# Performance work log

Measured on AMD Instinct MI355X. Metric: run time of the kernel, lower is better.

Reference implementation:

```python
import jax, jax.numpy as jnp
import numpy as np

HIDDEN = 1024
NUM_HEADS = 16
HEAD_DIM = HIDDEN // NUM_HEADS


def setup_inputs() -> dict:
    key = jax.random.key(0)
    ks = jax.random.split(key, 11)
    s = 1.0 / np.sqrt(HIDDEN)
    x = jax.random.normal(ks[0], (4, 2048, HIDDEN), dtype=jnp.float32)
    Wq = jax.random.uniform(ks[1], (HIDDEN, HIDDEN), jnp.float32, -s, s)
    bq = jax.random.uniform(ks[2], (HIDDEN,), jnp.float32, -s, s)
    Wk = jax.random.uniform(ks[3], (HIDDEN, HIDDEN), jnp.float32, -s, s)
    bk = jax.random.uniform(ks[4], (HIDDEN,), jnp.float32, -s, s)
    Wv = jax.random.uniform(ks[5], (HIDDEN, HIDDEN), jnp.float32, -s, s)
    bv = jax.random.uniform(ks[6], (HIDDEN,), jnp.float32, -s, s)
    Wo = jax.random.uniform(ks[7], (HIDDEN, HIDDEN), jnp.float32, -s, s)
    bo = jax.random.uniform(ks[8], (HIDDEN,), jnp.float32, -s, s)
    ln_g = jnp.ones((HIDDEN,), jnp.float32)
    ln_b = jnp.zeros((HIDDEN,), jnp.float32)
    return {"x": x, "Wq": Wq, "bq": bq, "Wk": Wk, "bk": bk,
            "Wv": Wv, "bv": bv, "Wo": Wo, "bo": bo,
            "ln_g": ln_g, "ln_b": ln_b}


def _layer_norm(x, g, b, eps=1e-5):
    mu = jnp.mean(x, axis=-1, keepdims=True)
    var = jnp.var(x, axis=-1, keepdims=True)
    return (x - mu) * jax.lax.rsqrt(var + eps) * g + b


def reference(x, Wq, bq, Wk, bk, Wv, bv, Wo, bo, ln_g, ln_b):
    B, S, _ = x.shape
    residual = x
    h = _layer_norm(x, ln_g, ln_b)
    # projections (torch Linear: y = h @ W.T + b)
    q = (h @ Wq.T + bq).reshape(B, S, NUM_HEADS, HEAD_DIM).transpose(0, 2, 1, 3)
    k = (h @ Wk.T + bk).reshape(B, S, NUM_HEADS, HEAD_DIM).transpose(0, 2, 1, 3)
    v = (h @ Wv.T + bv).reshape(B, S, NUM_HEADS, HEAD_DIM).transpose(0, 2, 1, 3)
    scores = jnp.einsum('bhqd,bhkd->bhqk', q, k) / np.sqrt(HEAD_DIM).astype(np.float32)
    weights = jax.nn.softmax(scores, axis=-1)  # dropout = identity (eval mode)
    context = jnp.einsum('bhqk,bhkd->bhqd', weights, v)
    context = context.transpose(0, 2, 1, 3).reshape(B, S, HIDDEN)
    out = context @ Wo.T + bo
    return out + residual
```

## Files before the change

kernel.cpp:

```cpp
#include <hip/hip_runtime.h>

typedef unsigned short u16;
typedef unsigned int   u32;
using bf16x8 = __attribute__((ext_vector_type(8))) __bf16;
using f32x4  = __attribute__((ext_vector_type(4))) float;
using u32x2  = __attribute__((ext_vector_type(2))) unsigned int;

__device__ __forceinline__ u16 f2b(float f){
  union { float f; u32 i; } v; v.f = f;
  u32 r = v.i + 0x7FFFu + ((v.i >> 16) & 1u);
  return (u16)(r >> 16);
}
__device__ __forceinline__ u32 pk_bf16_trunc(float a, float b){
  return __builtin_amdgcn_perm(__float_as_uint(b), __float_as_uint(a), 0x07060302u);
}

__global__ __launch_bounds__(256) void pre_kernel(const float* __restrict__ x, const float* __restrict__ g,
                                                  const float* __restrict__ be, u16* __restrict__ h,
                                                  const float* __restrict__ s0, const float* __restrict__ s1,
                                                  const float* __restrict__ s2, const float* __restrict__ s3,
                                                  u16* __restrict__ wd){
  const int tid = threadIdx.x;
  if (blockIdx.x >= 8192){
    const int b2 = blockIdx.x - 8192;
    const float* srcs[4] = {s0, s1, s2, s3};
    const float* s = srcs[b2 >> 10];
    u16* dd = wd + (size_t)(b2 >> 10) * (1024u * 1024u);
    const int i = ((b2 & 1023) * 256 + tid) * 4;
    float4 v = *(const float4*)(s + i);
    uint2 o;
    o.x = (u32)f2b(v.x) | ((u32)f2b(v.y) << 16);
    o.y = (u32)f2b(v.z) | ((u32)f2b(v.w) << 16);
    *(uint2*)(dd + i) = o;
    return;
  }
  const int row = blockIdx.x;
  const float* xr = x + (size_t)row * 1024u;
  float4 raw = *(const float4*)(xr + tid * 4);
  float s  = raw.x + raw.y + raw.z + raw.w;
  float sq = raw.x*raw.x + raw.y*raw.y + raw.z*raw.z + raw.w*raw.w;
  #pragma unroll
  for (int m = 1; m < 64; m <<= 1){ s += __shfl_xor(s, m); sq += __shfl_xor(sq, m); }
  __shared__ float ws[4], wq[4];
  if ((tid & 63) == 0){ ws[tid >> 6] = s; wq[tid >> 6] = sq; }
  __syncthreads();
  s  = ws[0] + ws[1] + ws[2] + ws[3];
  sq = wq[0] + wq[1] + wq[2] + wq[3];
  const float mu = s * (1.0f / 1024.0f);
  const float rstd = rsqrtf(sq * (1.0f / 1024.0f) - mu * mu + 1e-5f);
  float4 gg = *(const float4*)(g + tid * 4);
  float4 bb = *(const float4*)(be + tid * 4);
  float y0 = (raw.x - mu) * rstd * gg.x + bb.x;
  float y1 = (raw.y - mu) * rstd * gg.y + bb.y;
  float y2 = (raw.z - mu) * rstd * gg.z + bb.z;
  float y3 = (raw.w - mu) * rstd * gg.w + bb.w;
  uint2 outv;
  outv.x = (u32)f2b(y0) | ((u32)f2b(y1) << 16);
  outv.y = (u32)f2b(y2) | ((u32)f2b(y3) << 16);
  *(uint2*)(h + (size_t)row * 1024u + tid * 4) = outv;
}

__global__ __launch_bounds__(256) void gemm_qkv(const u16* __restrict__ A, const u16* __restrict__ Wcat,
                                                const float* __restrict__ bq, const float* __restrict__ bk,
                                                const float* __restrict__ bv,
                                                u16* __restrict__ qo, u16* __restrict__ ko, u16* __restrict__ vt){
  __shared__ u16 lA[2][4096];
  __shared__ u16 lB[2][4096];
  const int tid = threadIdx.x;
  const int lane = tid & 63, wv = tid >> 6, l15 = lane & 15, quad = lane >> 4;
  const int wr = wv >> 1, wc = wv & 1;
  const int row0 = blockIdx.x * 128, col0 = blockIdx.y * 128;
  const int K = 1024;

  const int r0_ = tid >> 2,         c0_ = tid & 3;
  const int r1_ = (256 + tid) >> 2, c1_ = (256 + tid) & 3;
  const u16* Asrc0 = A    + (size_t)(row0 + r0_) * K + (c0_ ^ ((r0_ >> 1) & 3)) * 8;
  const u16* Asrc1 = A    + (size_t)(row0 + r1_) * K + (c1_ ^ ((r1_ >> 1) & 3)) * 8;
  const u16* Bsrc0 = Wcat + (size_t)(col0 + r0_) * K + (c0_ ^ ((r0_ >> 1) & 3)) * 8;
  const u16* Bsrc1 = Wcat + (size_t)(col0 + r1_) * K + (c1_ ^ ((r1_ >> 1) & 3)) * 8;
  const int cr = (quad ^ ((l15 >> 1) & 3)) * 8;

  f32x4 acc[4][4] = {};
  uint4 ar0, ar1, br0, br1;
  ar0 = *(const uint4*)(Asrc0);
  ar1 = *(const uint4*)(Asrc1);
  br0 = *(const uint4*)(Bsrc0);
  br1 = *(const uint4*)(Bsrc1);
  *(uint4*)&lA[0][tid * 8] = ar0;
  *(uint4*)&lA[0][(256 + tid) * 8] = ar1;
  *(uint4*)&lB[0][tid * 8] = br0;
  *(uint4*)&lB[0][(256 + tid) * 8] = br1;
  ar0 = *(const uint4*)(Asrc0 + 32);
  ar1 = *(const uint4*)(Asrc1 + 32);
  br0 = *(const uint4*)(Bsrc0 + 32);
  br1 = *(const uint4*)(Bsrc1 + 32);
  __syncthreads();

  for (int kt = 0; kt < 32; ++kt){
    const int cur = kt & 1;
    if (kt < 31){
      *(uint4*)&lA[cur ^ 1][tid * 8] = ar0;
      *(uint4*)&lA[cur ^ 1][(256 + tid) * 8] = ar1;
      *(uint4*)&lB[cur ^ 1][tid * 8] = br0;
      *(uint4*)&lB[cur ^ 1][(256 + tid) * 8] = br1;
    }
    if (kt < 30){
      const int o = (kt + 2) * 32;
      ar0 = *(const uint4*)(Asrc0 + o);
      ar1 = *(const uint4*)(Asrc1 + o);
      br0 = *(const uint4*)(Bsrc0 + o);
      br1 = *(const uint4*)(Bsrc1 + o);
    }
    bf16x8 af[4], bf[4];
    #pragma unroll
    for (int i = 0; i < 4; ++i) af[i] = *(const bf16x8*)&lA[cur][(wr * 64 + i * 16 + l15) * 32 + cr];
    #pragma unroll
    for (int j = 0; j < 4; ++j) bf[j] = *(const bf16x8*)&lB[cur][(wc * 64 + j * 16 + l15) * 32 + cr];
    #pragma unroll
    for (int i = 0; i < 4; ++i)
      #pragma unroll
      for (int j = 0; j < 4; ++j)
        acc[i][j] = __builtin_amdgcn_mfma_f32_16x16x32_bf16(af[i], bf[j], acc[i][j], 0, 0, 0);
    __syncthreads();
  }
  const int sel = col0 >> 10;
  if (sel < 2){
    const float* bias = (sel == 0) ? bq : bk;
    u16* dst = (sel == 0) ? qo : ko;
    #pragma unroll
    for (int i = 0; i < 4; ++i){
      const int grow = row0 + wr * 64 + i * 16 + quad * 4;
      #pragma unroll
      for (int j = 0; j < 4; ++j){
        const int gcol = (col0 & 1023) + wc * 64 + j * 16 + l15;
        const float bb = bias[gcol];
        #pragma unroll
        for (int r = 0; r < 4; ++r){
          size_t off = (size_t)(grow + r) * 1024u + gcol;
          dst[off] = f2b(acc[i][j][r] + bb);
        }
      }
    }
  } else {
    u16* pw = &lA[0][0] + wv * 2048;
    const int bglob = row0 >> 11;
    const int head  = ((col0 & 1023) >> 6) + wc;
    const int srem0 = (row0 & 2047) + wr * 64;
    const size_t vbase = (size_t)((bglob * 16 + head) * 64) * 2048u;
    #pragma unroll
    for (int p = 0; p < 2; ++p){
      #pragma unroll
      for (int i2 = 0; i2 < 2; ++i2){
        const int i = p * 2 + i2;
        #pragma unroll
        for (int j = 0; j < 4; ++j){
          const int d = j * 16 + l15;
          const float bv_ = bv[(col0 & 1023) + wc * 64 + d];
          const int u = (i2 * 4 + quad) ^ (d & 7);
          uint2 pk;
          pk.x = (u32)f2b(acc[i][j][0] + bv_) | ((u32)f2b(acc[i][j][1] + bv_) << 16);
          pk.y = (u32)f2b(acc[i][j][2] + bv_) | ((u32)f2b(acc[i][j][3] + bv_) << 16);
          *(uint2*)&pw[d * 32 + u * 4] = pk;
        }
      }
      const int dl = lane;
      #pragma unroll
      for (int c = 0; c < 4; ++c){
        const int u0 = (2 * c) ^ (dl & 7), u1 = (2 * c + 1) ^ (dl & 7);
        uint2 lo = *(const uint2*)&pw[dl * 32 + u0 * 4];
        uint2 hi = *(const uint2*)&pw[dl * 32 + u1 * 4];
        uint4 o4; o4.x = lo.x; o4.y = lo.y; o4.z = hi.x; o4.w = hi.y;
        *(uint4*)(vt + vbase + (size_t)dl * 2048u + srem0 + p * 32 + c * 8) = o4;
      }
    }
  }
}

__global__ __launch_bounds__(256) void gemm_out(const u16* __restrict__ A, const u16* __restrict__ W,
                                                const float* __restrict__ bias, const float* __restrict__ res,
                                                float* __restrict__ C, int M, int N, int K){
  __shared__ u16 lA[2][4096];
  __shared__ u16 lB[2][4096];
  const int tid = threadIdx.x;
  const int lane = tid & 63, wv = tid >> 6, l15 = lane & 15, quad = lane >> 4;
  const int wr = wv >> 1, wc = wv & 1;
  const int row0 = blockIdx.x * 128, col0 = blockIdx.y * 128;

  const int r0_ = tid >> 2,         c0_ = tid & 3;
  const int r1_ = (256 + tid) >> 2, c1_ = (256 + tid) & 3;
  const u16* Asrc0 = A + (size_t)(row0 + r0_) * K + (c0_ ^ ((r0_ >> 1) & 3)) * 8;
  const u16* Asrc1 = A + (size_t)(row0 + r1_) * K + (c1_ ^ ((r1_ >> 1) & 3)) * 8;
  const u16* Bsrc0 = W + (size_t)(col0 + r0_) * K + (c0_ ^ ((r0_ >> 1) & 3)) * 8;
  const u16* Bsrc1 = W + (size_t)(col0 + r1_) * K + (c1_ ^ ((r1_ >> 1) & 3)) * 8;
  const int cr = (quad ^ ((l15 >> 1) & 3)) * 8;

  f32x4 acc[4][4] = {};
  const int nkt = K >> 5;
  uint4 ar0, ar1, br0, br1;
  ar0 = *(const uint4*)(Asrc0);
  ar1 = *(const uint4*)(Asrc1);
  br0 = *(const uint4*)(Bsrc0);
  br1 = *(const uint4*)(Bsrc1);
  *(uint4*)&lA[0][tid * 8] = ar0;
  *(uint4*)&lA[0][(256 + tid) * 8] = ar1;
  *(uint4*)&lB[0][tid * 8] = br0;
  *(uint4*)&lB[0][(256 + tid) * 8] = br1;
  ar0 = *(const uint4*)(Asrc0 + 32);
  ar1 = *(const uint4*)(Asrc1 + 32);
  br0 = *(const uint4*)(Bsrc0 + 32);
  br1 = *(const uint4*)(Bsrc1 + 32);
  __syncthreads();

  for (int kt = 0; kt < nkt; ++kt){
    const int cur = kt & 1;
    if (kt < nkt - 1){
      *(uint4*)&lA[cur ^ 1][tid * 8] = ar0;
      *(uint4*)&lA[cur ^ 1][(256 + tid) * 8] = ar1;
      *(uint4*)&lB[cur ^ 1][tid * 8] = br0;
      *(uint4*)&lB[cur ^ 1][(256 + tid) * 8] = br1;
    }
    if (kt < nkt - 2){
      const int o = (kt + 2) * 32;
      ar0 = *(const uint4*)(Asrc0 + o);
      ar1 = *(const uint4*)(Asrc1 + o);
      br0 = *(const uint4*)(Bsrc0 + o);
      br1 = *(const uint4*)(Bsrc1 + o);
    }
    bf16x8 af[4], bf[4];
    #pragma unroll
    for (int i = 0; i < 4; ++i) af[i] = *(const bf16x8*)&lA[cur][(wr * 64 + i * 16 + l15) * 32 + cr];
    #pragma unroll
    for (int j = 0; j < 4; ++j) bf[j] = *(const bf16x8*)&lB[cur][(wc * 64 + j * 16 + l15) * 32 + cr];
    #pragma unroll
    for (int i = 0; i < 4; ++i)
      #pragma unroll
      for (int j = 0; j < 4; ++j)
        acc[i][j] = __builtin_amdgcn_mfma_f32_16x16x32_bf16(af[i], bf[j], acc[i][j], 0, 0, 0);
    __syncthreads();
  }
  #pragma unroll
  for (int i = 0; i < 4; ++i){
    const int grow = row0 + wr * 64 + i * 16 + quad * 4;
    #pragma unroll
    for (int j = 0; j < 4; ++j){
      const int gcol = col0 + wc * 64 + j * 16 + l15;
      const float bb = bias[gcol];
      #pragma unroll
      for (int r = 0; r < 4; ++r){
        size_t off = (size_t)(grow + r) * N + gcol;
        C[off] = acc[i][j][r] + bb + res[off];
      }
    }
  }
}

__global__ __launch_bounds__(256, 2) void attn_kernel(const u16* __restrict__ Q, const u16* __restrict__ K,
                                                      const u16* __restrict__ Vt, u16* __restrict__ O){
  __shared__ u16 kls[2][64 * 64];
  __shared__ u16 vls[2][64 * 64];
  const int tid = threadIdx.x;
  const int lane = tid & 63, wv = tid >> 6, l15 = lane & 15, quad = lane >> 4;
  const int bh = blockIdx.x & 63, qt = blockIdx.x >> 6;
  const int b = bh >> 4, hh = bh & 15;
  const int q0 = qt * 256;
  const u16* Qg = Q + ((size_t)b * 2048u) * 1024u + hh * 64;
  const u16* Kg = K + ((size_t)b * 2048u) * 1024u + hh * 64;
  const u16* Vg = Vt + (size_t)bh * 64u * 2048u;
  u16* Og = O + ((size_t)b * 2048u) * 1024u + hh * 64;

  const int sr = tid >> 3, sc = tid & 7, sr2 = sr + 32;
  const int sx = (sc ^ (sr & 7)) * 8;
  const int c0 = ((quad ^ (l15 & 7))) * 8;

  const float QSCALE = 0.125f * 1.44269504f;
  bf16x8 qf2[4][2];
  #pragma unroll
  for (int g = 0; g < 4; ++g)
    #pragma unroll
    for (int kk = 0; kk < 2; ++kk){
      qf2[g][kk] = *(const bf16x8*)(Qg + (size_t)(q0 + wv * 64 + g * 16 + l15) * 1024u + kk * 32 + quad * 8);
      #pragma unroll
      for (int e = 0; e < 8; ++e) qf2[g][kk][e] = (__bf16)((float)qf2[g][kk][e] * QSCALE);
    }

  bf16x8 ones_f;
  {
    const __bf16 onev = (__bf16)1.0f, zerov = (__bf16)0.0f;
    #pragma unroll
    for (int e = 0; e < 8; ++e) ones_f[e] = (l15 == 0) ? onev : zerov;
  }

  f32x4 o2[4][4] = {};
  f32x4 o_l[4] = {};
  const f32x4 zf = {0.f, 0.f, 0.f, 0.f};

  uint4 kr0, kr1, vr0, vr1;
  kr0 = *(const uint4*)(Kg + (size_t)sr  * 1024u + sc * 8);
  vr0 = *(const uint4*)(Vg + (size_t)sr  * 2048u + sc * 8);
  kr1 = *(const uint4*)(Kg + (size_t)sr2 * 1024u + sc * 8);
  vr1 = *(const uint4*)(Vg + (size_t)sr2 * 2048u + sc * 8);
  *(uint4*)&kls[0][sr  * 64 + sx] = kr0;
  *(uint4*)&vls[0][sr  * 64 + sx] = vr0;
  *(uint4*)&kls[0][sr2 * 64 + sx] = kr1;
  *(uint4*)&vls[0][sr2 * 64 + sx] = vr1;
  kr0 = *(const uint4*)(Kg + (size_t)(64 + sr)  * 1024u + sc * 8);
  vr0 = *(const uint4*)(Vg + (size_t)sr  * 2048u + 64 + sc * 8);
  kr1 = *(const uint4*)(Kg + (size_t)(64 + sr2) * 1024u + sc * 8);
  vr1 = *(const uint4*)(Vg + (size_t)sr2 * 2048u + 64 + sc * 8);
  __syncthreads();

  for (int kt = 0; kt < 32; ++kt){
    const int cur = kt & 1;
    const u16* kb = kls[cur];
    const u16* vb = vls[cur];
    if (kt < 31){
      u16* kw = kls[cur ^ 1];
      u16* vw = vls[cur ^ 1];
      *(uint4*)&kw[sr  * 64 + sx] = kr0;
      *(uint4*)&vw[sr  * 64 + sx] = vr0;
      *(uint4*)&kw[sr2 * 64 + sx] = kr1;
      *(uint4*)&vw[sr2 * 64 + sx] = vr1;
    }
    if (kt < 30){
      const int s0 = (kt + 2) * 64;
      kr0 = *(const uint4*)(Kg + (size_t)(s0 + sr)  * 1024u + sc * 8);
      vr0 = *(const uint4*)(Vg + (size_t)sr  * 2048u + s0 + sc * 8);
      kr1 = *(const uint4*)(Kg + (size_t)(s0 + sr2) * 1024u + sc * 8);
      vr1 = *(const uint4*)(Vg + (size_t)sr2 * 2048u + s0 + sc * 8);
    }

    f32x4 s2[4][4];
    #pragma unroll
    for (int j = 0; j < 4; ++j){
      const int rb = (j * 16 + l15) * 64;
      bf16x8 kfr0 = *(const bf16x8*)&kb[rb + c0];
      bf16x8 kfr1 = *(const bf16x8*)&kb[rb + (c0 ^ 32)];
      #pragma unroll
      for (int g = 0; g < 4; ++g){
        f32x4 a = __builtin_amdgcn_mfma_f32_16x16x32_bf16(kfr0, qf2[g][0], zf, 0, 0, 0);
        s2[g][j] = __builtin_amdgcn_mfma_f32_16x16x32_bf16(kfr1, qf2[g][1], a, 0, 0, 0);
      }
    }

    #pragma unroll
    for (int g = 0; g < 4; ++g)
      #pragma unroll
      for (int j = 0; j < 4; ++j)
        #pragma unroll
        for (int r = 0; r < 4; ++r)
          s2[g][j][r] = __builtin_amdgcn_exp2f(s2[g][j][r]);

    #pragma unroll
    for (int kk = 0; kk < 2; ++kk){
      bf16x8 afr[4];
      #pragma unroll
      for (int g = 0; g < 4; ++g){
        const int j0 = kk * 2, j1 = j0 + 1;
        u32 A0 = pk_bf16_trunc(s2[g][j0][0], s2[g][j0][1]);
        u32 A1 = pk_bf16_trunc(s2[g][j0][2], s2[g][j0][3]);
        u32 B0 = pk_bf16_trunc(s2[g][j1][0], s2[g][j1][1]);
        u32 B1 = pk_bf16_trunc(s2[g][j1][2], s2[g][j1][3]);
        u32x2 r1 = __builtin_amdgcn_permlane32_swap(A0, B0, false, false);
        u32x2 r2 = __builtin_amdgcn_permlane16_swap(r1[0], r1[1], false, false);
        u32x2 r3 = __builtin_amdgcn_permlane32_swap(A1, B1, false, false);
        u32x2 r4 = __builtin_amdgcn_permlane16_swap(r3[0], r3[1], false, false);
        union { uint4 u; bf16x8 v; } cv;
        cv.u.x = r2[0]; cv.u.y = r4[0]; cv.u.z = r2[1]; cv.u.w = r4[1];
        afr[g] = cv.v;
      }
      #pragma unroll
      for (int g = 0; g < 4; ++g)
        o_l[g] = __builtin_amdgcn_mfma_f32_16x16x32_bf16(afr[g], ones_f, o_l[g], 0, 0, 0);
      #pragma unroll
      for (int j2 = 0; j2 < 4; ++j2){
        bf16x8 bfr = *(const bf16x8*)&vb[(j2 * 16 + l15) * 64 + (c0 ^ (kk * 32))];
        #pragma unroll
        for (int g = 0; g < 4; ++g)
          o2[g][j2] = __builtin_amdgcn_mfma_f32_16x16x32_bf16(afr[g], bfr, o2[g][j2], 0, 0, 0);
      }
    }
    __syncthreads();
  }

  #pragma unroll
  for (int g = 0; g < 4; ++g){
    float lr[4];
    #pragma unroll
    for (int r = 0; r < 4; ++r) lr[r] = 1.0f / __shfl(o_l[g][r], quad * 16);
    #pragma unroll
    for (int j2 = 0; j2 < 4; ++j2){
      #pragma unroll
      for (int r = 0; r < 4; ++r){
        const int qrow = q0 + wv * 64 + g * 16 + quad * 4 + r;
        const int d = j2 * 16 + l15;
        Og[(size_t)qrow * 1024u + d] = f2b(o2[g][j2][r] * lr[r]);
      }
    }
  }
}

extern "C" void kernel_launch(void* const* d_in, const int* in_sizes, int n_in,
                              void* d_out, int out_size, void* d_ws, size_t ws_size,
                              hipStream_t stream){
  (void)in_sizes; (void)n_in; (void)out_size; (void)ws_size;
  const float* x   = (const float*)d_in[0];
  const float* Wq  = (const float*)d_in[1];
  const float* bq  = (const float*)d_in[2];
  const float* Wk  = (const float*)d_in[3];
  const float* bk  = (const float*)d_in[4];
  const float* Wv  = (const float*)d_in[5];
  const float* bv  = (const float*)d_in[6];
  const float* Wo  = (const float*)d_in[7];
  const float* bo  = (const float*)d_in[8];
  const float* lng = (const float*)d_in[9];
  const float* lnb = (const float*)d_in[10];
  float* out = (float*)d_out;

  const size_t TE = (size_t)8192 * 1024;
  u16* ws0 = (u16*)d_ws;
  u16* ws1 = ws0 + TE;
  u16* ws2 = ws1 + TE;
  u16* wsw = ws2 + TE;
  u16* wob = wsw + (size_t)3 * 1024 * 1024;
  u16* vt  = (u16*)d_out;

  pre_kernel<<<dim3(12288), 256, 0, stream>>>(x, lng, lnb, ws0, Wq, Wk, Wv, Wo, wsw);
  gemm_qkv<<<dim3(64, 24), 256, 0, stream>>>(ws0, wsw, bq, bk, bv, ws1, ws2, vt);
  attn_kernel<<<dim3(512), 256, 0, stream>>>(ws1, ws2, vt, ws1);
  gemm_out<<<dim3(64, 8), 256, 0, stream>>>(ws1, wob, bo, x, out, 8192, 1024, 1024);
}
```

Before: 264.6 us.

## Process two K/V tiles per barrier in attention with quad-buffered LDS

```diff
diff --git a/kernel.cpp b/kernel.cpp
--- a/kernel.cpp
+++ b/kernel.cpp
@@ -256,8 +256,8 @@
 
 __global__ __launch_bounds__(256, 2) void attn_kernel(const u16* __restrict__ Q, const u16* __restrict__ K,
                                                       const u16* __restrict__ Vt, u16* __restrict__ O){
-  __shared__ u16 kls[2][64 * 64];
-  __shared__ u16 vls[2][64 * 64];
+  __shared__ u16 kls[4][64 * 64];
+  __shared__ u16 vls[4][64 * 64];
   const int tid = threadIdx.x;
   const int lane = tid & 63, wv = tid >> 6, l15 = lane & 15, quad = lane >> 4;
   const int bh = blockIdx.x & 63, qt = blockIdx.x >> 6;
@@ -294,93 +294,114 @@
   f32x4 o_l[4] = {};
   const f32x4 zf = {0.f, 0.f, 0.f, 0.f};
 
-  uint4 kr0, kr1, vr0, vr1;
-  kr0 = *(const uint4*)(Kg + (size_t)sr  * 1024u + sc * 8);
-  vr0 = *(const uint4*)(Vg + (size_t)sr  * 2048u + sc * 8);
-  kr1 = *(const uint4*)(Kg + (size_t)sr2 * 1024u + sc * 8);
-  vr1 = *(const uint4*)(Vg + (size_t)sr2 * 2048u + sc * 8);
-  *(uint4*)&kls[0][sr  * 64 + sx] = kr0;
-  *(uint4*)&vls[0][sr  * 64 + sx] = vr0;
-  *(uint4*)&kls[0][sr2 * 64 + sx] = kr1;
-  *(uint4*)&vls[0][sr2 * 64 + sx] = vr1;
-  kr0 = *(const uint4*)(Kg + (size_t)(64 + sr)  * 1024u + sc * 8);
-  vr0 = *(const uint4*)(Vg + (size_t)sr  * 2048u + 64 + sc * 8);
-  kr1 = *(const uint4*)(Kg + (size_t)(64 + sr2) * 1024u + sc * 8);
-  vr1 = *(const uint4*)(Vg + (size_t)sr2 * 2048u + 64 + sc * 8);
+#define ATTN_TILE(KB, VB) { \
+    f32x4 s2[4][4]; \
+    _Pragma("unroll") \
+    for (int j = 0; j < 4; ++j){ \
+      const int rb = (j * 16 + l15) * 64; \
+      bf16x8 kfr0 = *(const bf16x8*)&(KB)[rb + c0]; \
+      bf16x8 kfr1 = *(const bf16x8*)&(KB)[rb + (c0 ^ 32)]; \
+      _Pragma("unroll") \
+      for (int g = 0; g < 4; ++g){ \
+        f32x4 a = __builtin_amdgcn_mfma_f32_16x16x32_bf16(kfr0, qf2[g][0], zf, 0, 0, 0); \
+        s2[g][j] = __builtin_amdgcn_mfma_f32_16x16x32_bf16(kfr1, qf2[g][1], a, 0, 0, 0); \
+      } \
+    } \
+    _Pragma("unroll") \
+    for (int g = 0; g < 4; ++g) \
+      _Pragma("unroll") \
+      for (int j = 0; j < 4; ++j) \
+        _Pragma("unroll") \
+        for (int r = 0; r < 4; ++r) \
+          s2[g][j][r] = __builtin_amdgcn_exp2f(s2[g][j][r]); \
+    _Pragma("unroll") \
+    for (int kk = 0; kk < 2; ++kk){ \
+      bf16x8 afr[4]; \
+      _Pragma("unroll") \
+      for (int g = 0; g < 4; ++g){ \
+        const int j0 = kk * 2, j1 = j0 + 1; \
+        u32 A0 = pk_bf16_trunc(s2[g][j0][0], s2[g][j0][1]); \
+        u32 A1 = pk_bf16_trunc(s2[g][j0][2], s2[g][j0][3]); \
+        u32 B0 = pk_bf16_trunc(s2[g][j1][0], s2[g][j1][1]); \
+        u32 B1 = pk_bf16_trunc(s2[g][j1][2], s2[g][j1][3]); \
+        u32x2 r1 = __builtin_amdgcn_permlane32_swap(A0, B0, false, false); \
+        u32x2 r2 = __builtin_amdgcn_permlane16_swap(r1[0], r1[1], false, false); \
+        u32x2 r3 = __builtin_amdgcn_permlane32_swap(A1, B1, false, false); \
+        u32x2 r4 = __builtin_amdgcn_permlane16_swap(r3[0], r3[1], false, false); \
+        union { uint4 u; bf16x8 v; } cv; \
+        cv.u.x = r2[0]; cv.u.y = r4[0]; cv.u.z = r2[1]; cv.u.w = r4[1]; \
+        afr[g] = cv.v; \
+      } \
+      _Pragma("unroll") \
+      for (int g = 0; g < 4; ++g) \
+        o_l[g] = __builtin_amdgcn_mfma_f32_16x16x32_bf16(afr[g], ones_f, o_l[g], 0, 0, 0); \
+      _Pragma("unroll") \
+      for (int j2 = 0; j2 < 4; ++j2){ \
+        bf16x8 bfr = *(const bf16x8*)&(VB)[(j2 * 16 + l15) * 64 + (c0 ^ (kk * 32))]; \
+        _Pragma("unroll") \
+        for (int g = 0; g < 4; ++g) \
+          o2[g][j2] = __builtin_amdgcn_mfma_f32_16x16x32_bf16(afr[g], bfr, o2[g][j2], 0, 0, 0); \
+      } \
+    } \
+  }
+
+  uint4 kA0, kA1, vA0, vA1, kB0, kB1, vB0, vB1;
+  kA0 = *(const uint4*)(Kg + (size_t)sr  * 1024u + sc * 8);
+  vA0 = *(const uint4*)(Vg + (size_t)sr  * 2048u + sc * 8);
+  kA1 = *(const uint4*)(Kg + (size_t)sr2 * 1024u + sc * 8);
+  vA1 = *(const uint4*)(Vg + (size_t)sr2 * 2048u + sc * 8);
+  kB0 = *(const uint4*)(Kg + (size_t)(64 + sr)  * 1024u + sc * 8);
+  vB0 = *(const uint4*)(Vg + (size_t)sr  * 2048u + 64 + sc * 8);
+  kB1 = *(const uint4*)(Kg + (size_t)(64 + sr2) * 1024u + sc * 8);
+  vB1 = *(const uint4*)(Vg + (size_t)sr2 * 2048u + 64 + sc * 8);
+  *(uint4*)&kls[0][sr  * 64 + sx] = kA0;
+  *(uint4*)&vls[0][sr  * 64 + sx] = vA0;
+  *(uint4*)&kls[0][sr2 * 64 + sx] = kA1;
+  *(uint4*)&vls[0][sr2 * 64 + sx] = vA1;
+  *(uint4*)&kls[1][sr  * 64 + sx] = kB0;
+  *(uint4*)&vls[1][sr  * 64 + sx] = vB0;
+  *(uint4*)&kls[1][sr2 * 64 + sx] = kB1;
+  *(uint4*)&vls[1][sr2 * 64 + sx] = vB1;
+  kA0 = *(const uint4*)(Kg + (size_t)(128 + sr)  * 1024u + sc * 8);
+  vA0 = *(const uint4*)(Vg + (size_t)sr  * 2048u + 128 + sc * 8);
+  kA1 = *(const uint4*)(Kg + (size_t)(128 + sr2) * 1024u + sc * 8);
+  vA1 = *(const uint4*)(Vg + (size_t)sr2 * 2048u + 128 + sc * 8);
+  kB0 = *(const uint4*)(Kg + (size_t)(192 + sr)  * 1024u + sc * 8);
+  vB0 = *(const uint4*)(Vg + (size_t)sr  * 2048u + 192 + sc * 8);
+  kB1 = *(const uint4*)(Kg + (size_t)(192 + sr2) * 1024u + sc * 8);
+  vB1 = *(const uint4*)(Vg + (size_t)sr2 * 2048u + 192 + sc * 8);
   __syncthreads();
 
-  for (int kt = 0; kt < 32; ++kt){
-    const int cur = kt & 1;
-    const u16* kb = kls[cur];
-    const u16* vb = vls[cur];
-    if (kt < 31){
-      u16* kw = kls[cur ^ 1];
-      u16* vw = vls[cur ^ 1];
-      *(uint4*)&kw[sr  * 64 + sx] = kr0;
-      *(uint4*)&vw[sr  * 64 + sx] = vr0;
-      *(uint4*)&kw[sr2 * 64 + sx] = kr1;
-      *(uint4*)&vw[sr2 * 64 + sx] = vr1;
-    }
-    if (kt < 30){
-      const int s0 = (kt + 2) * 64;
-      kr0 = *(const uint4*)(Kg + (size_t)(s0 + sr)  * 1024u + sc * 8);
-      vr0 = *(const uint4*)(Vg + (size_t)sr  * 2048u + s0 + sc * 8);
-      kr1 = *(const uint4*)(Kg + (size_t)(s0 + sr2) * 1024u + sc * 8);
-      vr1 = *(const uint4*)(Vg + (size_t)sr2 * 2048u + s0 + sc * 8);
-    }
-
-    f32x4 s2[4][4];
-    #pragma unroll
-    for (int j = 0; j < 4; ++j){
-      const int rb = (j * 16 + l15) * 64;
-      bf16x8 kfr0 = *(const bf16x8*)&kb[rb + c0];
-      bf16x8 kfr1 = *(const bf16x8*)&kb[rb + (c0 ^ 32)];
-      #pragma unroll
-      for (int g = 0; g < 4; ++g){
-        f32x4 a = __builtin_amdgcn_mfma_f32_16x16x32_bf16(kfr0, qf2[g][0], zf, 0, 0, 0);
-        s2[g][j] = __builtin_amdgcn_mfma_f32_16x16x32_bf16(kfr1, qf2[g][1], a, 0, 0, 0);
-      }
-    }
-
-    #pragma unroll
-    for (int g = 0; g < 4; ++g)
-      #pragma unroll
-      for (int j = 0; j < 4; ++j)
-        #pragma unroll
-        for (int r = 0; r < 4; ++r)
-          s2[g][j][r] = __builtin_amdgcn_exp2f(s2[g][j][r]);
-
-    #pragma unroll
-    for (int kk = 0; kk < 2; ++kk){
-      bf16x8 afr[4];
-      #pragma unroll
-      for (int g = 0; g < 4; ++g){
-        const int j0 = kk * 2, j1 = j0 + 1;
-        u32 A0 = pk_bf16_trunc(s2[g][j0][0], s2[g][j0][1]);
-        u32 A1 = pk_bf16_trunc(s2[g][j0][2], s2[g][j0][3]);
-        u32 B0 = pk_bf16_trunc(s2[g][j1][0], s2[g][j1][1]);
-        u32 B1 = pk_bf16_trunc(s2[g][j1][2], s2[g][j1][3]);
-        u32x2 r1 = __builtin_amdgcn_permlane32_swap(A0, B0, false, false);
-        u32x2 r2 = __builtin_amdgcn_permlane16_swap(r1[0], r1[1], false, false);
-        u32x2 r3 = __builtin_amdgcn_permlane32_swap(A1, B1, false, false);
-        u32x2 r4 = __builtin_amdgcn_permlane16_swap(r3[0], r3[1], false, false);
-        union { uint4 u; bf16x8 v; } cv;
-        cv.u.x = r2[0]; cv.u.y = r4[0]; cv.u.z = r2[1]; cv.u.w = r4[1];
-        afr[g] = cv.v;
-      }
-      #pragma unroll
-      for (int g = 0; g < 4; ++g)
-        o_l[g] = __builtin_amdgcn_mfma_f32_16x16x32_bf16(afr[g], ones_f, o_l[g], 0, 0, 0);
-      #pragma unroll
-      for (int j2 = 0; j2 < 4; ++j2){
-        bf16x8 bfr = *(const bf16x8*)&vb[(j2 * 16 + l15) * 64 + (c0 ^ (kk * 32))];
-        #pragma unroll
-        for (int g = 0; g < 4; ++g)
-          o2[g][j2] = __builtin_amdgcn_mfma_f32_16x16x32_bf16(afr[g], bfr, o2[g][j2], 0, 0, 0);
-      }
-    }
+  for (int it = 0; it < 16; ++it){
+    const int e = (it & 1) << 1;
+    if (it < 15){
+      u16* kw0 = kls[e ^ 2]; u16* vw0 = vls[e ^ 2];
+      u16* kw1 = kls[(e ^ 2) + 1]; u16* vw1 = vls[(e ^ 2) + 1];
+      *(uint4*)&kw0[sr  * 64 + sx] = kA0;
+      *(uint4*)&vw0[sr  * 64 + sx] = vA0;
+      *(uint4*)&kw0[sr2 * 64 + sx] = kA1;
+      *(uint4*)&vw0[sr2 * 64 + sx] = vA1;
+      *(uint4*)&kw1[sr  * 64 + sx] = kB0;
+      *(uint4*)&vw1[sr  * 64 + sx] = vB0;
+      *(uint4*)&kw1[sr2 * 64 + sx] = kB1;
+      *(uint4*)&vw1[sr2 * 64 + sx] = vB1;
+    }
+    if (it < 14){
+      const int sA = (2 * it + 4) * 64, sB = (2 * it + 5) * 64;
+      kA0 = *(const uint4*)(Kg + (size_t)(sA + sr)  * 1024u + sc * 8);
+      vA0 = *(const uint4*)(Vg + (size_t)sr  * 2048u + sA + sc * 8);
+      kA1 = *(const uint4*)(Kg + (size_t)(sA + sr2) * 1024u + sc * 8);
+      vA1 = *(const uint4*)(Vg + (size_t)sr2 * 2048u + sA + sc * 8);
+      kB0 = *(const uint4*)(Kg + (size_t)(sB + sr)  * 1024u + sc * 8);
+      vB0 = *(const uint4*)(Vg + (size_t)sr  * 2048u + sB + sc * 8);
+      kB1 = *(const uint4*)(Kg + (size_t)(sB + sr2) * 1024u + sc * 8);
+      vB1 = *(const uint4*)(Vg + (size_t)sr2 * 2048u + sB + sc * 8);
+    }
+    { const u16* kbuf = kls[e];     const u16* vbuf = vls[e];     ATTN_TILE(kbuf, vbuf); }
+    { const u16* kbuf = kls[e + 1]; const u16* vbuf = vls[e + 1]; ATTN_TILE(kbuf, vbuf); }
     __syncthreads();
   }
+#undef ATTN_TILE
 
   #pragma unroll
   for (int g = 0; g < 4; ++g){
```

Result: no change. 269.2 us (+1.7%).
